# Optimization experiments

Hardware: AMD Instinct MI355X
Metric: run time of the kernel (lower is better)

Reference implementation:

```python
import jax, jax.numpy as jnp
import numpy as np

H = 12  # num_heads

def _attn(q, k, v):
    sim = jnp.einsum('bid,bjd->bij', q, k)
    a = jax.nn.softmax(sim, axis=-1)
    return jnp.einsum('bij,bjd->bid', a, v)

def _layernorm(x, g, b, eps=1e-5):
    mu = x.mean(-1, keepdims=True)
    var = ((x - mu) ** 2).mean(-1, keepdims=True)
    return (x - mu) * jax.lax.rsqrt(var + eps) * g + b

def setup_inputs() -> dict:
    key = jax.random.key(0)
    ks = jax.random.split(key, 8)
    B, F, NP, D, DT, NT = 8, 8, 196, 768, 512, 77
    N = 1 + F * NP
    s = 0.02
    return {
        'x': jax.random.normal(ks[0], (B, N, D), jnp.float32),
        'y': jax.random.normal(ks[1], (B, NT, DT), jnp.float32),
        'y_mask': jnp.zeros((B, NT), jnp.float32),
        'f': F,
        'w_qkv': jax.random.normal(ks[2], (D, 3 * D), jnp.float32) * s,
        'w_proj': jax.random.normal(ks[3], (D, D), jnp.float32) * s,
        'b_proj': jnp.zeros((D,), jnp.float32),
        'w_kv_text': jax.random.normal(ks[4], (DT, 2 * D), jnp.float32) * s,
        'w_q_i2t': jax.random.normal(ks[5], (D, D), jnp.float32) * s,
        'w_proj_i2t': jax.random.normal(ks[6], (D, D), jnp.float32) * s,
        'b_proj_i2t': jnp.zeros((D,), jnp.float32),
        'alpha_i2t': jnp.full((1,), 0.1, jnp.float32),
        'ln_g': jnp.ones((D,), jnp.float32),
        'ln_b': jnp.zeros((D,), jnp.float32),
    }

def reference(x, y, y_mask, f, w_qkv, w_proj, b_proj, w_kv_text, w_q_i2t,
              w_proj_i2t, b_proj_i2t, alpha_i2t, ln_g, ln_b):
    B, N, D = x.shape
    d = D // H
    scale = d ** -0.5
    qkv = x @ w_qkv  # [B, N, 3D]
    q, k, v = jnp.split(qkv, 3, axis=-1)
    to_bh = lambda t: t.reshape(B, N, H, d).transpose(0, 2, 1, 3).reshape(B * H, N, d)
    q, k, v = map(to_bh, (q, k, v))
    q = q * scale
    cls_q, q_ = q[:, :1], q[:, 1:]
    cls_k, k_ = k[:, :1], k[:, 1:]
    cls_v, v_ = v[:, :1], v[:, 1:]
    # cls token attends to everything
    cls_out = _attn(cls_q, k, v)  # [B*H, 1, d]
    # divided space attention: 'b (f n) d -> (b f) n d'
    n = (N - 1) // f
    split_f = lambda t: t.reshape(B * H * f, n, d)
    q_, k_, v_ = map(split_f, (q_, k_, v_))
    rep = lambda t: jnp.broadcast_to(t[:, None], (B * H, f, 1, d)).reshape(B * H * f, 1, d)
    k_ = jnp.concatenate([rep(cls_k), k_], axis=1)  # [B*H*f, n+1, d]
    v_ = jnp.concatenate([rep(cls_v), v_], axis=1)
    out = _attn(q_, k_, v_).reshape(B * H, N - 1, d)
    out = jnp.concatenate([cls_out, out], axis=1)  # [B*H, N, d]
    out = out.reshape(B, H, N, d).transpose(0, 2, 1, 3).reshape(B, N, D)
    x_out = out @ w_proj + b_proj
    # image-to-text cross attention
    NT = y.shape[1]
    kv = (y @ w_kv_text).reshape(B, NT, 2, H, d).transpose(2, 0, 3, 1, 4)
    k_t, v_t = kv[0], kv[1]  # [B, H, NT, d]
    q_i = (_layernorm(x_out, ln_g, ln_b) @ w_q_i2t).reshape(B, N, H, d).transpose(0, 2, 1, 3)
    q_i = q_i * (d ** -0.5)
    a = jnp.einsum('bhnd,bhmd->bhnm', q_i, k_t) + y_mask[:, None, None, :]
    a = jax.nn.softmax(a, axis=-1)
    yo = jnp.einsum('bhnm,bhmd->bhnd', a, v_t).transpose(0, 2, 1, 3).reshape(B, N, D)
    yo = yo @ w_proj_i2t + b_proj_i2t
    return x_out + alpha_i2t * yo
```

## Files before the change

kernel.cpp:

```cpp
#include <hip/hip_runtime.h>

typedef __bf16 bf16x8 __attribute__((ext_vector_type(8)));
typedef float f32x4 __attribute__((ext_vector_type(4)));
typedef unsigned short us_t;

#define DEV __device__ __forceinline__

DEV float bf2f(unsigned short u) {
  union { unsigned int i; float f; } c; c.i = ((unsigned int)u) << 16; return c.f;
}
DEV unsigned short f2bf(float f) {
  union { float f; unsigned int i; } c; c.f = f;
  return (unsigned short)((c.i + 0x7FFFu + ((c.i >> 16) & 1u)) >> 16);
}
DEV unsigned int cvt_pk_bf16(float lo, float hi) {
  unsigned int r;
  asm("v_cvt_pk_bf16_f32 %0, %1, %2" : "=v"(r) : "v"(lo), "v"(hi));
  return r;
}

union FragU { bf16x8 v; unsigned short u[8]; };

DEV void gld_lds16(const void* g, void* l) {
  __builtin_amdgcn_global_load_lds((const __attribute__((address_space(1))) void*)g,
                                   (__attribute__((address_space(3))) void*)l, 16, 0, 0);
}

#define MFMA(a, b, c) __builtin_amdgcn_mfma_f32_16x16x32_bf16((a), (b), (c), 0, 0, 0)

#define BB 8
#define NN 1569
#define DD 768
#define HH 12
#define DH 64
#define FF 8
#define NFR 196
#define NTT 77
#define DT_ 512
#define MROWS 12552
#define MTEXT 616

__global__ void cvt_fused(const float* __restrict__ xin, unsigned short* __restrict__ xout, int n4x,
                          const float* __restrict__ yin, unsigned short* __restrict__ yout, int n4y) {
  int i = blockIdx.x * blockDim.x + threadIdx.x;
  int stride = gridDim.x * blockDim.x;
  int total = n4x + n4y;
  for (; i < total; i += stride) {
    const float4* src; ushort4* dst; int idx;
    if (i < n4x) { src = (const float4*)xin; dst = (ushort4*)xout; idx = i; }
    else         { src = (const float4*)yin; dst = (ushort4*)yout; idx = i - n4x; }
    float4 v = src[idx];
    ushort4 o;
    o.x = f2bf(v.x); o.y = f2bf(v.y); o.z = f2bf(v.z); o.w = f2bf(v.w);
    dst[idx] = o;
  }
}

struct TJobs {
  const float* in[5];
  unsigned short* out[5];
  int R[5], C[5];
};

__global__ __launch_bounds__(256) void transpose_all(TJobs j) {
  __shared__ float tile[32][33];
  int z = blockIdx.z;
  int R = j.R[z], C = j.C[z];
  int bx = blockIdx.x * 32;
  int by = blockIdx.y * 32;
  if (bx >= C || by >= R) return;
  const float* in = j.in[z];
  unsigned short* out = j.out[z];
  int tx = threadIdx.x & 31;
  int ty0 = threadIdx.x >> 5;
  for (int dy = 0; dy < 32; dy += 8) {
    int r = by + ty0 + dy, c = bx + tx;
    tile[ty0 + dy][tx] = (r < R && c < C) ? in[(size_t)r * C + c] : 0.f;
  }
  __syncthreads();
  for (int dy = 0; dy < 32; dy += 8) {
    int orow = bx + ty0 + dy;
    int ocol = by + tx;
    if (orow < C && ocol < R) out[(size_t)orow * R + ocol] = f2bf(tile[tx][ty0 + dy]);
  }
}

enum { EPI_QKV = 0, EPI_XOUT = 1, EPI_QI = 2, EPI_KVT = 3, EPI_FINAL = 4 };

struct EpiParams {
  float* outf;
  unsigned short *o0, *o1, *o2;
  const float *bias, *aux, *alphap;
};

template <int EPI>
__global__ __launch_bounds__(256)
void gemm_bt(const unsigned short* __restrict__ A, const unsigned short* __restrict__ Bt,
             int M, int K, EpiParams ep) {
  __shared__ __align__(16) unsigned short lA[128 * 32];
  __shared__ __align__(16) unsigned short lB[128 * 32];
  const int nbx = gridDim.x, nwg = gridDim.x * gridDim.y;
  int flat = blockIdx.y * nbx + blockIdx.x;
  {
    int q = nwg >> 3, r = nwg & 7;
    int xcd = flat & 7, i = flat >> 3;
    flat = (xcd < r ? xcd * (q + 1) : r * (q + 1) + (xcd - r) * q) + i;
  }
  const int brow = (flat / nbx) * 128, bcol = (flat % nbx) * 128;
  const int t = threadIdx.x, wave = t >> 6, lane = t & 63, g = lane >> 4, l15 = lane & 15;
  const int wr = wave >> 1, wc = wave & 1;

  f32x4 acc[4][4];
#pragma unroll
  for (int i = 0; i < 4; ++i)
#pragma unroll
    for (int j = 0; j < 4; ++j) acc[i][j] = {0.f, 0.f, 0.f, 0.f};

  const int nk = K >> 5;
  for (int kt = 0; kt < nk; ++kt) {
    const int k0 = kt << 5;
#pragma unroll
    for (int c = 0; c < 2; ++c) {
      int sb = wave * 1024 + c * 512;
      int slot = sb + lane * 8;
      int row = slot >> 5;
      int gl = (slot >> 3) & 3;
      int swz = gl ^ ((row >> 1) & 3);
      int ra = brow + row; if (ra > M - 1) ra = M - 1;
      gld_lds16(A + (size_t)ra * K + k0 + swz * 8, &lA[sb]);
      int rb = bcol + row;
      gld_lds16(Bt + (size_t)rb * K + k0 + swz * 8, &lB[sb]);
    }
    __syncthreads();
    FragU af[4], bf[4];
#pragma unroll
    for (int i = 0; i < 4; ++i) {
      int rowa = wr * 64 + i * 16 + l15;
      int swa = g ^ ((rowa >> 1) & 3);
      af[i].v = *(const bf16x8*)(&lA[rowa * 32 + swa * 8]);
      int rowb = wc * 64 + i * 16 + l15;
      int swb = g ^ ((rowb >> 1) & 3);
      bf[i].v = *(const bf16x8*)(&lB[rowb * 32 + swb * 8]);
    }
#pragma unroll
    for (int i = 0; i < 4; ++i)
#pragma unroll
      for (int j = 0; j < 4; ++j)
        acc[i][j] = MFMA(af[i].v, bf[j].v, acc[i][j]);
    __syncthreads();
  }

#pragma unroll
  for (int i = 0; i < 4; ++i) {
#pragma unroll
    for (int r = 0; r < 4; ++r) {
      int mrow = brow + wr * 64 + i * 16 + g * 4 + r;
      if (mrow >= M) continue;
      int bidx = 0, nn = 0, tt = 0;
      if constexpr (EPI == EPI_QKV || EPI == EPI_QI) { bidx = mrow / NN; nn = mrow - bidx * NN; }
      if constexpr (EPI == EPI_KVT) { bidx = mrow / NTT; tt = mrow - bidx * NTT; }
#pragma unroll
      for (int j = 0; j < 4; ++j) {
        int col = bcol + wc * 64 + j * 16 + l15;
        float val = acc[i][j][r];
        if constexpr (EPI == EPI_XOUT) {
          ep.outf[(size_t)mrow * DD + col] = val + ep.bias[col];
        } else if constexpr (EPI == EPI_FINAL) {
          size_t o = (size_t)mrow * DD + col;
          ep.outf[o] = ep.aux[o] + ep.alphap[0] * (val + ep.bias[col]);
        } else if constexpr (EPI == EPI_QKV) {
          int which = col / DD; int within = col - which * DD;
          int h = within >> 6, dd2 = within & 63;
          size_t dstp = (((size_t)bidx * HH + h) * NN + nn) * DH + dd2;
          if (which == 0) ep.o0[dstp] = f2bf(val * 0.125f);
          else if (which == 1) ep.o1[dstp] = f2bf(val);
          else ep.o2[dstp] = f2bf(val);
        } else if constexpr (EPI == EPI_QI) {
          int h = col >> 6, dd2 = col & 63;
          ep.o0[(((size_t)bidx * HH + h) * NN + nn) * DH + dd2] = f2bf(val * 0.125f);
        } else if constexpr (EPI == EPI_KVT) {
          int kvi = col / DD; int within = col - kvi * DD;
          int h = within >> 6, dd2 = within & 63;
          size_t dstp = (((size_t)bidx * HH + h) * NTT + tt) * DH + dd2;
          if (kvi == 0) ep.o0[dstp] = f2bf(val);
          else ep.o1[dstp] = f2bf(val);
        }
      }
    }
  }
}

__global__ __launch_bounds__(256)
void attn_all(const unsigned short* __restrict__ qg, const unsigned short* __restrict__ kg,
              const unsigned short* __restrict__ vg, unsigned short* __restrict__ outg) {
  __shared__ __align__(16) char smem[224 * 64 * 2 + 64 * 232 * 2];
  const int t = threadIdx.x, lane = t & 63, g = lane >> 4, l15 = lane & 15;
  const int wave = t >> 6;

  if (blockIdx.x < 768) {
    unsigned short* lK = (unsigned short*)smem;
    unsigned short* lV = (unsigned short*)(smem + 224 * 64 * 2);
    const int bid = blockIdx.x, bh = bid >> 3, fi = bid & 7;
    const int b = bh / HH, h = bh - b * HH;
    const size_t base = (size_t)bh * NN * DH;

#pragma unroll
    for (int c = 0; c < 7; ++c) {
      int gI = t + 256 * c;
      int elem = gI * 8, row = elem >> 6, gl = (elem >> 3) & 7;
      int srcg = gl ^ (row & 7);
      int rr = row < 197 ? row : 196;
      int nrow = (rr == 0) ? 0 : (fi * NFR + rr);
      gld_lds16(kg + base + (size_t)nrow * DH + srcg * 8, &lK[elem]);
    }
    {
      float4 vreg[7]; int vkey[7], ve[7];
#pragma unroll
      for (int c = 0; c < 7; ++c) {
        int gI = t + 256 * c;
        if (gI < 1576) {
          int key = gI >> 3, e = gI & 7;
          int nrow = (key == 0) ? 0 : (fi * NFR + key);
          vreg[c] = *(const float4*)(vg + base + (size_t)nrow * DH + e * 8);
          vkey[c] = key; ve[c] = e;
        }
      }
#pragma unroll
      for (int c = 0; c < 7; ++c) {
        int gI = t + 256 * c;
        if (gI < 1576) {
          const unsigned short* u = (const unsigned short*)&vreg[c];
          int d0 = ve[c] * 8, key = vkey[c];
#pragma unroll
          for (int z = 0; z < 8; ++z) lV[(d0 + z) * 232 + key] = u[z];
        }
      }
      for (int idx = t; idx < 27 * 64; idx += 256) {
        int key = 197 + (idx >> 6), dd = idx & 63;
        lV[dd * 232 + key] = 0;
      }
    }
    __syncthreads();

    for (int qt = wave; qt < 13; qt += 4) {
      int qr = qt * 16 + l15; if (qr > 195) qr = 195;
      const unsigned short* qp = qg + base + (size_t)(1 + fi * NFR + qr) * DH + g * 8;
      bf16x8 bq0 = *(const bf16x8*)(qp);
      bf16x8 bq1 = *(const bf16x8*)(qp + 32);
      f32x4 s[13];
#pragma unroll
      for (int kt2 = 0; kt2 < 13; ++kt2) {
        int krow = kt2 * 16 + l15;
        int rb = krow * 64;
        int sw0 = (g ^ (krow & 7)) * 8;
        int sw1 = ((4 + g) ^ (krow & 7)) * 8;
        f32x4 a = {0.f, 0.f, 0.f, 0.f};
        a = MFMA(*(const bf16x8*)(&lK[rb + sw0]), bq0, a);
        a = MFMA(*(const bf16x8*)(&lK[rb + sw1]), bq1, a);
        s[kt2] = a;
      }
      float m = -1e30f;
#pragma unroll
      for (int kt2 = 0; kt2 < 13; ++kt2)
#pragma unroll
        for (int r = 0; r < 4; ++r) {
          int key = kt2 * 16 + g * 4 + r;
          if (key >= 197) s[kt2][r] = -1e30f;
          m = fmaxf(m, s[kt2][r]);
        }
      m = fmaxf(m, __shfl_xor(m, 16));
      m = fmaxf(m, __shfl_xor(m, 32));
      float sum = 0.f;
#pragma unroll
      for (int kt2 = 0; kt2 < 13; ++kt2)
#pragma unroll
        for (int r = 0; r < 4; ++r) { float p = __expf(s[kt2][r] - m); s[kt2][r] = p; sum += p; }
      sum += __shfl_xor(sum, 16);
      sum += __shfl_xor(sum, 32);
      float inv = 1.f / sum;
#pragma unroll
      for (int kt2 = 0; kt2 < 13; ++kt2)
#pragma unroll
        for (int r = 0; r < 4; ++r) s[kt2][r] *= inv;
      unsigned int pk2[13][2];
#pragma unroll
      for (int c2 = 0; c2 < 13; ++c2) {
        pk2[c2][0] = cvt_pk_bf16(s[c2][0], s[c2][1]);
        pk2[c2][1] = cvt_pk_bf16(s[c2][2], s[c2][3]);
      }
      f32x4 o[4];
#pragma unroll
      for (int dt = 0; dt < 4; ++dt) o[dt] = {0.f, 0.f, 0.f, 0.f};
#pragma unroll
      for (int K32 = 0; K32 < 7; ++K32) {
        FragU af;
        unsigned int* aw = (unsigned int*)&af;
#pragma unroll
        for (int w = 0; w < 4; ++w) {
          int srcl = l15 + 16 * ((((lane >> 4) & 1) * 8 + 2 * w) >> 2);
          int v0 = __shfl((int)pk2[2 * K32][w & 1], srcl, 64);
          int v1 = (2 * K32 + 1 < 13) ? __shfl((int)pk2[2 * K32 + 1][w & 1], srcl, 64) : 0;
          aw[w] = (unsigned int)((g < 2) ? v0 : v1);
        }
#pragma unroll
        for (int dt = 0; dt < 4; ++dt) {
          const bf16x8 bv = *(const bf16x8*)(&lV[(dt * 16 + l15) * 232 + K32 * 32 + g * 8]);
          o[dt] = MFMA(af.v, bv, o[dt]);
        }
      }
#pragma unroll
      for (int dt = 0; dt < 4; ++dt)
#pragma unroll
        for (int r = 0; r < 4; ++r) {
          int qrow = qt * 16 + g * 4 + r;
          if (qrow < 196) {
            size_t nrow = 1 + (size_t)fi * NFR + qrow;
            outg[((size_t)b * NN + nrow) * DD + h * DH + dt * 16 + l15] = f2bf(o[dt][r]);
          }
        }
    }
  } else {
    float* q0 = (float*)smem;
    float* sc = (float*)(smem + 256);
    float* red = (float*)(smem + 256 + NN * 4);
    float* opart2 = (float*)(smem + 256 + NN * 4 + 1024);
    const int bh = blockIdx.x - 768, b = bh / HH, h = bh - b * HH;
    const size_t base = (size_t)bh * NN * DH;
    if (t < 64) q0[t] = bf2f(qg[base + t]);
    __syncthreads();
    for (int j = t; j < NN; j += 256) {
      const unsigned short* kr = kg + base + (size_t)j * DH;
      float s = 0.f;
#pragma unroll
      for (int dd = 0; dd < 64; dd += 8) {
        float4 raw = *(const float4*)(kr + dd);
        const unsigned short* pu = (const unsigned short*)&raw;
#pragma unroll
        for (int z = 0; z < 8; ++z) s += q0[dd + z] * bf2f(pu[z]);
      }
      sc[j] = s;
    }
    __syncthreads();
    float lm = -1e30f;
    for (int j = t; j < NN; j += 256) lm = fmaxf(lm, sc[j]);
    red[t] = lm; __syncthreads();
    for (int off = 128; off > 0; off >>= 1) { if (t < off) red[t] = fmaxf(red[t], red[t + off]); __syncthreads(); }
    float m = red[0];
    __syncthreads();
    float ls = 0.f;
    for (int j = t; j < NN; j += 256) { float p = __expf(sc[j] - m); sc[j] = p; ls += p; }
    __syncthreads();
    red[t] = ls; __syncthreads();
    for (int off = 128; off > 0; off >>= 1) { if (t < off) red[t] += red[t + off]; __syncthreads(); }
    float invS = 1.f / red[0];
    int jg = t >> 3, db = t & 7;
    float o8[8];
#pragma unroll
    for (int z = 0; z < 8; ++z) o8[z] = 0.f;
    for (int j = jg; j < NN; j += 32) {
      float sj = sc[j];
      float4 raw = *(const float4*)(vg + base + (size_t)j * DH + db * 8);
      const unsigned short* pu = (const unsigned short*)&raw;
#pragma unroll
      for (int z = 0; z < 8; ++z) o8[z] += sj * bf2f(pu[z]);
    }
#pragma unroll
    for (int z = 0; z < 8; ++z) opart2[jg * 66 + db * 8 + z] = o8[z];
    __syncthreads();
    if (t < 64) {
      float r = 0.f;
      for (int p2 = 0; p2 < 32; ++p2) r += opart2[p2 * 66 + t];
      outg[((size_t)b * NN) * DD + h * DH + t] = f2bf(r * invS);
    }
  }
}

__global__ __launch_bounds__(256)
void i2t_attn(const unsigned short* __restrict__ qg, const unsigned short* __restrict__ ktg,
              const unsigned short* __restrict__ vtg, const float* __restrict__ mask,
              unsigned short* __restrict__ outg) {
  __shared__ __align__(16) unsigned short lK[80 * 64];
  __shared__ __align__(16) unsigned short lV[64 * 104];
  const int bid = blockIdx.x;
  const int bh = bid % 96, chunk = bid / 96;
  const int b = bh / HH, h = bh - b * HH;
  const int t = threadIdx.x, wave = t >> 6, lane = t & 63, g = lane >> 4, l15 = lane & 15;
  const size_t kvbase = (size_t)bh * NTT * DH;
#pragma unroll
  for (int c = 0; c < 3; ++c) {
    int gI = t + 256 * c;
    if (gI < 640) {
      int elem = gI * 8, row = elem >> 6, gl = (elem >> 3) & 7;
      int srcg = gl ^ (row & 7);
      int rr = row < NTT ? row : NTT - 1;
      gld_lds16(ktg + kvbase + (size_t)rr * DH + srcg * 8, &lK[elem]);
    }
  }
  {
    float4 vreg[3]; int vkey[3], ve[3];
#pragma unroll
    for (int c = 0; c < 3; ++c) {
      int gI = t + 256 * c;
      if (gI < 616) {
        int key = gI >> 3, e = gI & 7;
        vreg[c] = *(const float4*)(vtg + kvbase + (size_t)key * DH + e * 8);
        vkey[c] = key; ve[c] = e;
      }
    }
#pragma unroll
    for (int c = 0; c < 3; ++c) {
      int gI = t + 256 * c;
      if (gI < 616) {
        const unsigned short* u = (const unsigned short*)&vreg[c];
        int d0 = ve[c] * 8, key = vkey[c];
#pragma unroll
        for (int z = 0; z < 8; ++z) lV[(d0 + z) * 104 + key] = u[z];
      }
    }
    for (int idx = t; idx < 27 * 64; idx += 256) {
      int key = NTT + (idx >> 6), dd = idx & 63;
      lV[dd * 104 + key] = 0;
    }
  }
  __syncthreads();
  const size_t qbase = (size_t)bh * NN * DH;
#pragma unroll
  for (int i4 = 0; i4 < 4; ++i4) {
    int qt = chunk * 16 + i4 * 4 + wave;
    if (qt >= 99) continue;
    int qr = qt * 16 + l15; if (qr > NN - 1) qr = NN - 1;
    const unsigned short* qp = qg + qbase + (size_t)qr * DH + g * 8;
    bf16x8 bq0 = *(const bf16x8*)(qp);
    bf16x8 bq1 = *(const bf16x8*)(qp + 32);
    f32x4 s[5];
#pragma unroll
    for (int kt2 = 0; kt2 < 5; ++kt2) {
      int krow = kt2 * 16 + l15;
      int rb = krow * 64;
      int sw0 = (g ^ (krow & 7)) * 8;
      int sw1 = ((4 + g) ^ (krow & 7)) * 8;
      f32x4 a = {0.f, 0.f, 0.f, 0.f};
      a = MFMA(*(const bf16x8*)(&lK[rb + sw0]), bq0, a);
      a = MFMA(*(const bf16x8*)(&lK[rb + sw1]), bq1, a);
      s[kt2] = a;
    }
    float m = -1e30f;
#pragma unroll
    for (int kt2 = 0; kt2 < 5; ++kt2)
#pragma unroll
      for (int r = 0; r < 4; ++r) {
        int key = kt2 * 16 + g * 4 + r;
        if (key < NTT) s[kt2][r] += mask[b * NTT + key];
        else s[kt2][r] = -1e30f;
        m = fmaxf(m, s[kt2][r]);
      }
    m = fmaxf(m, __shfl_xor(m, 16));
    m = fmaxf(m, __shfl_xor(m, 32));
    float sum = 0.f;
#pragma unroll
    for (int kt2 = 0; kt2 < 5; ++kt2)
#pragma unroll
      for (int r = 0; r < 4; ++r) { float p = __expf(s[kt2][r] - m); s[kt2][r] = p; sum += p; }
    sum += __shfl_xor(sum, 16);
    sum += __shfl_xor(sum, 32);
    float inv = 1.f / sum;
#pragma unroll
    for (int kt2 = 0; kt2 < 5; ++kt2)
#pragma unroll
      for (int r = 0; r < 4; ++r) s[kt2][r] *= inv;
    unsigned int pk2[5][2];
#pragma unroll
    for (int c2 = 0; c2 < 5; ++c2) {
      pk2[c2][0] = cvt_pk_bf16(s[c2][0], s[c2][1]);
      pk2[c2][1] = cvt_pk_bf16(s[c2][2], s[c2][3]);
    }
    f32x4 o[4];
#pragma unroll
    for (int dt = 0; dt < 4; ++dt) o[dt] = {0.f, 0.f, 0.f, 0.f};
#pragma unroll
    for (int K32 = 0; K32 < 3; ++K32) {
      FragU af;
      unsigned int* aw = (unsigned int*)&af;
#pragma unroll
      for (int w = 0; w < 4; ++w) {
        int srcl = l15 + 16 * ((((lane >> 4) & 1) * 8 + 2 * w) >> 2);
        int v0 = __shfl((int)pk2[2 * K32][w & 1], srcl, 64);
        int v1 = (2 * K32 + 1 < 5) ? __shfl((int)pk2[2 * K32 + 1][w & 1], srcl, 64) : 0;
        aw[w] = (unsigned int)((g < 2) ? v0 : v1);
      }
#pragma unroll
      for (int dt = 0; dt < 4; ++dt) {
        const bf16x8 bv = *(const bf16x8*)(&lV[(dt * 16 + l15) * 104 + K32 * 32 + g * 8]);
        o[dt] = MFMA(af.v, bv, o[dt]);
      }
    }
#pragma unroll
    for (int dt = 0; dt < 4; ++dt)
#pragma unroll
      for (int r = 0; r < 4; ++r) {
        int qrow = qt * 16 + g * 4 + r;
        if (qrow < NN)
          outg[((size_t)b * NN + qrow) * DD + h * DH + dt * 16 + l15] = f2bf(o[dt][r]);
      }
  }
}

__global__ __launch_bounds__(256)
void ln_kernel(const float* __restrict__ x, const float* __restrict__ gam,
               const float* __restrict__ bet, unsigned short* __restrict__ out) {
  __shared__ float red[256];
  const int row = blockIdx.x, t = threadIdx.x;
  const size_t base = (size_t)row * DD;
  float v0 = x[base + t], v1 = x[base + t + 256], v2 = x[base + t + 512];
  red[t] = v0 + v1 + v2; __syncthreads();
  for (int off = 128; off > 0; off >>= 1) { if (t < off) red[t] += red[t + off]; __syncthreads(); }
  float mu = red[0] * (1.f / 768.f);
  __syncthreads();
  float d0 = v0 - mu, d1 = v1 - mu, d2 = v2 - mu;
  red[t] = d0 * d0 + d1 * d1 + d2 * d2; __syncthreads();
  for (int off = 128; off > 0; off >>= 1) { if (t < off) red[t] += red[t + off]; __syncthreads(); }
  float rs = rsqrtf(red[0] * (1.f / 768.f) + 1e-5f);
  out[base + t] = f2bf(d0 * rs * gam[t] + bet[t]);
  out[base + t + 256] = f2bf(d1 * rs * gam[t + 256] + bet[t + 256]);
  out[base + t + 512] = f2bf(d2 * rs * gam[t + 512] + bet[t + 512]);
}

static constexpr size_t SZ_WQKVT = (size_t)2304 * 768 * 2;
static constexpr size_t SZ_W768  = (size_t)768 * 768 * 2;
static constexpr size_t SZ_WKVT  = (size_t)1536 * 512 * 2;
static constexpr size_t SZ_XB    = (size_t)MROWS * DD * 2;
static constexpr size_t SZ_YB    = (size_t)MTEXT * DT_ * 2;
static constexpr size_t SZ_KT    = (size_t)96 * NTT * DH * 2;

static constexpr size_t OFF_WQKVT = 0;
static constexpr size_t OFF_WPROJT = OFF_WQKVT + SZ_WQKVT;
static constexpr size_t OFF_WKVT = OFF_WPROJT + SZ_W768;
static constexpr size_t OFF_WQIT = OFF_WKVT + SZ_WKVT;
static constexpr size_t OFF_WPIT = OFF_WQIT + SZ_W768;
static constexpr size_t OFF_XB  = OFF_WPIT + SZ_W768;
static constexpr size_t OFF_YB  = OFF_XB + SZ_XB;
static constexpr size_t OFF_QB  = OFF_YB + SZ_YB;
static constexpr size_t OFF_KB  = OFF_QB + SZ_XB;
static constexpr size_t OFF_VB  = OFF_KB + SZ_XB;
static constexpr size_t OFF_XOUT = OFF_VB + SZ_XB;

extern "C" void kernel_launch(void* const* d_in, const int* in_sizes, int n_in,
                              void* d_out, int out_size, void* d_ws, size_t ws_size,
                              hipStream_t stream) {
  const float* x      = (const float*)d_in[0];
  const float* y      = (const float*)d_in[1];
  const float* y_mask = (const float*)d_in[2];
  const float* w_qkv  = (const float*)d_in[4];
  const float* w_proj = (const float*)d_in[5];
  const float* b_proj = (const float*)d_in[6];
  const float* w_kv   = (const float*)d_in[7];
  const float* w_qi   = (const float*)d_in[8];
  const float* w_pi   = (const float*)d_in[9];
  const float* b_pi   = (const float*)d_in[10];
  const float* alpha  = (const float*)d_in[11];
  const float* ln_g   = (const float*)d_in[12];
  const float* ln_b   = (const float*)d_in[13];
  float* out = (float*)d_out;
  char* ws = (char*)d_ws;

  us_t* wqkvT = (us_t*)(ws + OFF_WQKVT);
  us_t* wprojT = (us_t*)(ws + OFF_WPROJT);
  us_t* wkvT = (us_t*)(ws + OFF_WKVT);
  us_t* wqiT = (us_t*)(ws + OFF_WQIT);
  us_t* wpiT = (us_t*)(ws + OFF_WPIT);
  us_t* xb  = (us_t*)(ws + OFF_XB);
  us_t* yb  = (us_t*)(ws + OFF_YB);
  us_t* qb  = (us_t*)(ws + OFF_QB);
  us_t* kb  = (us_t*)(ws + OFF_KB);
  us_t* vb  = (us_t*)(ws + OFF_VB);
  float* xoutf = (float*)(ws + OFF_XOUT);
  us_t* attn_out = xb;
  us_t* lnout = qb;
  us_t* qib = kb;
  us_t* ktb = vb;
  us_t* vtb = (us_t*)(ws + OFF_VB + SZ_KT);
  us_t* i2t_out = xb;

  cvt_fused<<<2048, 256, 0, stream>>>(x, xb, MROWS * DD / 4, y, yb, MTEXT * DT_ / 4);
  TJobs tj;
  tj.in[0] = w_qkv;  tj.out[0] = wqkvT;  tj.R[0] = 768; tj.C[0] = 2304;
  tj.in[1] = w_proj; tj.out[1] = wprojT; tj.R[1] = 768; tj.C[1] = 768;
  tj.in[2] = w_kv;   tj.out[2] = wkvT;   tj.R[2] = 512; tj.C[2] = 1536;
  tj.in[3] = w_qi;   tj.out[3] = wqiT;   tj.R[3] = 768; tj.C[3] = 768;
  tj.in[4] = w_pi;   tj.out[4] = wpiT;   tj.R[4] = 768; tj.C[4] = 768;
  transpose_all<<<dim3(72, 24, 5), 256, 0, stream>>>(tj);

  EpiParams e1{}; e1.o0 = qb; e1.o1 = kb; e1.o2 = vb;
  gemm_bt<EPI_QKV><<<dim3(18, 99), 256, 0, stream>>>(xb, wqkvT, MROWS, 768, e1);

  attn_all<<<864, 256, 0, stream>>>(qb, kb, vb, attn_out);

  EpiParams e2{}; e2.outf = xoutf; e2.bias = b_proj;
  gemm_bt<EPI_XOUT><<<dim3(6, 99), 256, 0, stream>>>(attn_out, wprojT, MROWS, 768, e2);

  ln_kernel<<<MROWS, 256, 0, stream>>>(xoutf, ln_g, ln_b, lnout);

  EpiParams e3{}; e3.o0 = qib;
  gemm_bt<EPI_QI><<<dim3(6, 99), 256, 0, stream>>>(lnout, wqiT, MROWS, 768, e3);

  EpiParams e4{}; e4.o0 = ktb; e4.o1 = vtb;
  gemm_bt<EPI_KVT><<<dim3(12, 5), 256, 0, stream>>>(yb, wkvT, MTEXT, 512, e4);

  i2t_attn<<<dim3(96 * 7), 256, 0, stream>>>(qib, ktb, vtb, y_mask, i2t_out);

  EpiParams e5{}; e5.outf = out; e5.bias = b_pi; e5.aux = xoutf; e5.alphap = alpha;
  gemm_bt<EPI_FINAL><<<dim3(6, 99), 256, 0, stream>>>(i2t_out, wpiT, MROWS, 768, e5);
}
```

Baseline: 340.1 us.

## Triple-buffer LDS in GEMM with async prefetch two k-tiles ahead

Turns the single-buffered GEMM main loop into a three-stage LDS ring. Global-to-LDS loads for tile kt+2 are issued before computing tile kt, and explicit vmcnt waits with raw barriers replace __syncthreads. Load addresses are also hoisted out of the loop. The aim is to hide global memory latency behind the MFMA work, at the cost of three times the LDS footprint, which may reduce occupancy.

After: 332.9 us. -2.1%, faster.

```diff
diff --git a/kernel.cpp b/kernel.cpp
--- a/kernel.cpp
+++ b/kernel.cpp
@@ -97,8 +97,8 @@
 __global__ __launch_bounds__(256)
 void gemm_bt(const unsigned short* __restrict__ A, const unsigned short* __restrict__ Bt,
              int M, int K, EpiParams ep) {
-  __shared__ __align__(16) unsigned short lA[128 * 32];
-  __shared__ __align__(16) unsigned short lB[128 * 32];
+  __shared__ __align__(16) unsigned short lA[3][128 * 32];
+  __shared__ __align__(16) unsigned short lB[3][128 * 32];
   const int nbx = gridDim.x, nwg = gridDim.x * gridDim.y;
   int flat = blockIdx.y * nbx + blockIdx.x;
   {
@@ -110,6 +110,28 @@
   const int t = threadIdx.x, wave = t >> 6, lane = t & 63, g = lane >> 4, l15 = lane & 15;
   const int wr = wave >> 1, wc = wave & 1;
 
+  int dsto[2];
+  const unsigned short *pA[2], *pB[2];
+#pragma unroll
+  for (int c = 0; c < 2; ++c) {
+    int sb = wave * 1024 + c * 512;
+    int slot = sb + lane * 8;
+    int row = slot >> 5;
+    int gl = (slot >> 3) & 3;
+    int swz = gl ^ ((row >> 1) & 3);
+    int ra = brow + row; if (ra > M - 1) ra = M - 1;
+    dsto[c] = sb;
+    pA[c] = A + (size_t)ra * K + swz * 8;
+    pB[c] = Bt + (size_t)(bcol + row) * K + swz * 8;
+  }
+
+#define STG(s, k0) do { \
+    gld_lds16(pA[0] + (k0), &lA[s][dsto[0]]); \
+    gld_lds16(pB[0] + (k0), &lB[s][dsto[0]]); \
+    gld_lds16(pA[1] + (k0), &lA[s][dsto[1]]); \
+    gld_lds16(pB[1] + (k0), &lB[s][dsto[1]]); \
+    __builtin_amdgcn_sched_barrier(0); } while (0)
+
   f32x4 acc[4][4];
 #pragma unroll
   for (int i = 0; i < 4; ++i)
@@ -117,38 +139,41 @@
     for (int j = 0; j < 4; ++j) acc[i][j] = {0.f, 0.f, 0.f, 0.f};
 
   const int nk = K >> 5;
+  STG(0, 0);
+  if (nk > 1) STG(1, 32);
+
   for (int kt = 0; kt < nk; ++kt) {
-    const int k0 = kt << 5;
-#pragma unroll
-    for (int c = 0; c < 2; ++c) {
-      int sb = wave * 1024 + c * 512;
-      int slot = sb + lane * 8;
-      int row = slot >> 5;
-      int gl = (slot >> 3) & 3;
-      int swz = gl ^ ((row >> 1) & 3);
-      int ra = brow + row; if (ra > M - 1) ra = M - 1;
-      gld_lds16(A + (size_t)ra * K + k0 + swz * 8, &lA[sb]);
-      int rb = bcol + row;
-      gld_lds16(Bt + (size_t)rb * K + k0 + swz * 8, &lB[sb]);
-    }
-    __syncthreads();
+    const int s = kt % 3;
+    if (kt + 2 < nk) STG((kt + 2) % 3, (kt + 2) << 5);
+    if (kt + 2 < nk)      { asm volatile("s_waitcnt vmcnt(8)" ::: "memory"); }
+    else if (kt + 1 < nk) { asm volatile("s_waitcnt vmcnt(4)" ::: "memory"); }
+    else                  { asm volatile("s_waitcnt vmcnt(0)" ::: "memory"); }
+    __builtin_amdgcn_sched_barrier(0);
+    asm volatile("s_barrier" ::: "memory");
+    __builtin_amdgcn_sched_barrier(0);
+
     FragU af[4], bf[4];
 #pragma unroll
     for (int i = 0; i < 4; ++i) {
       int rowa = wr * 64 + i * 16 + l15;
       int swa = g ^ ((rowa >> 1) & 3);
-      af[i].v = *(const bf16x8*)(&lA[rowa * 32 + swa * 8]);
+      af[i].v = *(const bf16x8*)(&lA[s][rowa * 32 + swa * 8]);
       int rowb = wc * 64 + i * 16 + l15;
       int swb = g ^ ((rowb >> 1) & 3);
-      bf[i].v = *(const bf16x8*)(&lB[rowb * 32 + swb * 8]);
+      bf[i].v = *(const bf16x8*)(&lB[s][rowb * 32 + swb * 8]);
     }
 #pragma unroll
     for (int i = 0; i < 4; ++i)
 #pragma unroll
       for (int j = 0; j < 4; ++j)
         acc[i][j] = MFMA(af[i].v, bf[j].v, acc[i][j]);
-    __syncthreads();
-  }
+
+    asm volatile("s_waitcnt lgkmcnt(0)" ::: "memory");
+    __builtin_amdgcn_sched_barrier(0);
+    asm volatile("s_barrier" ::: "memory");
+    __builtin_amdgcn_sched_barrier(0);
+  }
+#undef STG
 
 #pragma unroll
   for (int i = 0; i < 4; ++i) {
```
